# Optimization experiments

Hardware: AMD Instinct MI355X
Metric: run time of the kernel (lower is better)

The kernel has to match this reference:

```python
import jax, jax.numpy as jnp
import numpy as np

BN_EPS = 1e-5


def _weight_mlp(off, Wh, bh, Wo, bo):
    # off: [Nout, k, 2] relative neighbor offsets -> [Nout, k, 9] interp coeffs
    h = jax.nn.relu(off @ Wh + bh)
    return h @ Wo + bo


def _interp_conv(x, idx, off, Wk, bk, Wh, bh, Wo, bo):
    # x: [B, Cin, Nin]; idx: [Nout, k] neighbor indices into Nin; Wk: [Cout, Cin, 9]
    a = _weight_mlp(off, Wh, bh, Wo, bo)        # [Nout, k, 9]
    feats = x[:, :, idx]                         # gather -> [B, Cin, Nout, k]
    # dynamic filter: per-neighbor kernel = a @ Wk taps, contracted with features
    y = jnp.einsum('nkt,bcnk,oct->bon', a, feats, Wk)  # [B, Cout, Nout]
    return y + bk[None, :, None]


def _bn_relu(x, g, b):
    # BatchNorm1d over [B, C, N] using batch statistics (training-mode forward)
    mean = x.mean(axis=(0, 2), keepdims=True)
    var = x.var(axis=(0, 2), keepdims=True)
    xn = (x - mean) * jax.lax.rsqrt(var + BN_EPS)
    return jax.nn.relu(xn * g[None, :, None] + b[None, :, None])


def setup_inputs() -> dict:
    key = jax.random.key(0)
    ks = jax.random.split(key, 12)
    B, N1, N2, N3, K = 8, 50176, 12544, 3136, 9
    inp = {
        'x': jax.random.normal(ks[0], (B, 3, N1), jnp.float32),
        'nbr1': jax.random.randint(ks[1], (N2, K), 0, N1, jnp.int32),
        'off1': jax.random.normal(ks[2], (N2, K, 2), jnp.float32),
        'nbr2': jax.random.randint(ks[3], (N2, K), 0, N2, jnp.int32),
        'off2': jax.random.normal(ks[4], (N2, K, 2), jnp.float32),
        'pool_idx': jax.random.randint(ks[5], (N3, K), 0, N2, jnp.int32),
        'Wh': jax.random.normal(ks[6], (2, 32), jnp.float32) * 0.5,
        'bh': jnp.zeros((32,), jnp.float32),
        'Wo': jax.random.normal(ks[7], (32, 9), jnp.float32) * 0.2,
        'bo': jnp.zeros((9,), jnp.float32),
        'W1': jax.random.normal(ks[8], (32, 3, 9), jnp.float32) * 0.2,
        'b1': jnp.zeros((32,), jnp.float32),
        'W2': jax.random.normal(ks[9], (32, 32, 9), jnp.float32) * 0.06,
        'b2': jnp.zeros((32,), jnp.float32),
        'W3': jax.random.normal(ks[10], (64, 32, 9), jnp.float32) * 0.06,
        'b3': jnp.zeros((64,), jnp.float32),
        'g1': jnp.ones((32,), jnp.float32), 'be1': jnp.zeros((32,), jnp.float32),
        'g2': jnp.ones((32,), jnp.float32), 'be2': jnp.zeros((32,), jnp.float32),
        'g3': jnp.ones((64,), jnp.float32), 'be3': jnp.zeros((64,), jnp.float32),
    }
    return inp


def reference(x, nbr1, off1, nbr2, off2, pool_idx, Wh, bh, Wo, bo,
              W1, b1, W2, b2, W3, b3, g1, be1, g2, be2, g3, be3):
    x = _bn_relu(_interp_conv(x, nbr1, off1, W1, b1, Wh, bh, Wo, bo), g1, be1)
    x = _bn_relu(_interp_conv(x, nbr2, off2, W2, b2, Wh, bh, Wo, bo), g2, be2)
    x = _bn_relu(_interp_conv(x, nbr2, off2, W3, b3, Wh, bh, Wo, bo), g3, be3)
    # MaxPoolNG: max over irregular neighbor sets from level l2 -> l3
    x = x[:, :, pool_idx].max(axis=-1)           # [B, 64, N3]
    return x
```

## Files before the change

### kernel.cpp

```cpp
#include <hip/hip_runtime.h>
#include <math.h>

#define N1C 50176
#define N2C 12544
#define N3C 3136
#define NT_TILES (N2C * 8 / 64)

typedef __attribute__((ext_vector_type(8))) short bf16x8;
typedef __attribute__((ext_vector_type(4))) float f32x4;
typedef __attribute__((ext_vector_type(2))) unsigned uint2v;

__device__ __forceinline__ unsigned short f2bf(float f) {
    unsigned u = __builtin_bit_cast(unsigned, f);
    u += 0x7fffu + ((u >> 16) & 1u);
    return (unsigned short)(u >> 16);
}
__device__ __forceinline__ unsigned packbf(float a, float b) {
    return (unsigned)f2bf(a) | ((unsigned)f2bf(b) << 16);
}
__device__ __forceinline__ float bf2f(unsigned short u) {
    return __builtin_bit_cast(float, (unsigned)u << 16);
}
__device__ __forceinline__ float bflo(unsigned u) {
    return __builtin_bit_cast(float, u << 16);
}
__device__ __forceinline__ float bfhi(unsigned u) {
    return __builtin_bit_cast(float, u & 0xffff0000u);
}

#define TRB (N1C / 64)
#define MLB (2 * N2C * 9 / 256)
#define PWB 112

__device__ __forceinline__ void pad_one(int i, const float* __restrict__ W,
                                        unsigned short* __restrict__ Wp,
                                        int OC, int CIN, int KT) {
    int j = i & 7;
    int op = (i >> 3) & 31;
    int q = (i >> 8) & 3;
    int kt = (i >> 10) % KT;
    int g = i / (KT * 1024);
    int kp = kt * 32 + q * 8 + j;
    int t = kp / CIN, c = kp - t * CIN;
    int o = g * 32 + op;
    float v = (t < 9 && o < OC) ? W[(o * CIN + c) * 9 + t] : 0.f;
    Wp[i] = f2bf(v);
}

__global__ void prologue_kernel(const float* __restrict__ x, unsigned short* __restrict__ X0,
                                const float* __restrict__ off1, const float* __restrict__ off2,
                                const float* __restrict__ Wh, const float* __restrict__ bh,
                                const float* __restrict__ Wo, const float* __restrict__ bo,
                                float* __restrict__ A1, float* __restrict__ A2,
                                const float* __restrict__ W1, const float* __restrict__ W2,
                                const float* __restrict__ W3,
                                unsigned short* __restrict__ W1p, unsigned short* __restrict__ W2p,
                                unsigned short* __restrict__ W3p) {
    __shared__ float T[64][25];
    int blk = blockIdx.x;
    int tid = threadIdx.x;
    if (blk < TRB) {
        int n0 = blk * 64;
        for (int r = tid; r < 24 * 64; r += 256) {
            int cb = r >> 6;
            int nn = r & 63;
            T[nn][cb] = x[cb * N1C + n0 + nn];
        }
        __syncthreads();
        for (int w = tid; w < 64 * 24; w += 256) {
            int nn = w / 24;
            int u = w - nn * 24;
            X0[(n0 + nn) * 24 + u] = f2bf(T[nn][u]);
        }
    } else if (blk < TRB + MLB) {
        int idx = (blk - TRB) * 256 + tid;
        const float* offp;
        float* Ap;
        if (idx < N2C * 9) { offp = off1 + idx * 2; Ap = A1 + idx * 9; }
        else { int i2 = idx - N2C * 9; offp = off2 + i2 * 2; Ap = A2 + i2 * 9; }
        float o0 = offp[0], o1 = offp[1];
        float out[9];
#pragma unroll
        for (int t = 0; t < 9; t++) out[t] = bo[t];
#pragma unroll
        for (int h = 0; h < 32; h++) {
            float hv = fmaxf(o0 * Wh[h] + o1 * Wh[32 + h] + bh[h], 0.f);
#pragma unroll
            for (int t = 0; t < 9; t++) out[t] += hv * Wo[h * 9 + t];
        }
#pragma unroll
        for (int t = 0; t < 9; t++) Ap[t] = out[t];
    } else {
        int i = (blk - TRB - MLB) * 256 + tid;
        if (i < 1024) pad_one(i, W1, W1p, 32, 3, 1);
        else if (i < 10240) pad_one(i - 1024, W2, W2p, 32, 32, 9);
        else pad_one(i - 10240, W3, W3p, 64, 32, 9);
    }
}

__global__ __launch_bounds__(256, 8)
void conv1_kernel(const unsigned short* __restrict__ Xin,
                  const int* __restrict__ nbr,
                  const float* __restrict__ A,
                  const unsigned short* __restrict__ Wp,
                  const float* __restrict__ bias,
                  unsigned short* __restrict__ Yb) {
    constexpr int KSTR = 40;
    __shared__ alignas(16) short S[64 * KSTR];
    int tid = threadIdx.x;
    int n0 = blockIdx.x * 8;
    for (int i = tid; i < 64 * KSTR; i += 256) S[i] = 0;
    __syncthreads();
    if (tid < 192) {
        int nsub = tid / 24;
        int u = tid - nsub * 24;
        int b = u / 3, c = u - b * 3;
        int n = n0 + nsub;
        const int* nb = nbr + n * 9;
        const float* Ar = A + n * 81;
        float f[9];
#pragma unroll
        for (int k = 0; k < 9; k++) f[k] = bf2f(Xin[nb[k] * 24 + u]);
        float s[9];
#pragma unroll
        for (int t = 0; t < 9; t++) s[t] = 0.f;
#pragma unroll
        for (int k = 0; k < 9; k++)
#pragma unroll
            for (int t = 0; t < 9; t++) s[t] = fmaf(Ar[k * 9 + t], f[k], s[t]);
        int col = nsub * 8 + b;
#pragma unroll
        for (int t = 0; t < 9; t++) S[col * KSTR + t * 3 + c] = (short)f2bf(s[t]);
    }
    __syncthreads();
    int lane = tid & 63, wv = tid >> 6, q = lane >> 4, cl = lane & 15;
    int colg = wv * 16 + cl;
    const bf16x8* wf = (const bf16x8*)Wp;
    f32x4 acc0 = {0.f, 0.f, 0.f, 0.f};
    f32x4 acc1 = {0.f, 0.f, 0.f, 0.f};
    bf16x8 bfr = *(const bf16x8*)&S[colg * KSTR + q * 8];
    bf16x8 a0 = wf[q * 32 + cl];
    bf16x8 a1 = wf[q * 32 + cl + 16];
    acc0 = __builtin_amdgcn_mfma_f32_16x16x32_bf16(a0, bfr, acc0, 0, 0, 0);
    acc1 = __builtin_amdgcn_mfma_f32_16x16x32_bf16(a1, bfr, acc1, 0, 0, 0);
    int C = blockIdx.x * 64 + colg;
#pragma unroll
    for (int m = 0; m < 2; m++) {
        f32x4 ac = m ? acc1 : acc0;
        int ob = m * 16 + q * 4;
        uint2v uu;
        uu.x = packbf(ac[0] + bias[ob + 0], ac[1] + bias[ob + 1]);
        uu.y = packbf(ac[2] + bias[ob + 2], ac[3] + bias[ob + 3]);
        *(uint2v*)&Yb[(size_t)C * 32 + ob] = uu;
    }
}

#define KSTR32 296

template <int MW, bool HAS_BN>
__global__ __launch_bounds__(256, 8)
void conv32_kernel(const unsigned short* __restrict__ Xin,
                   const int* __restrict__ nbr,
                   const float* __restrict__ A,
                   const unsigned short* __restrict__ Wp,
                   const float* __restrict__ bias,
                   const float* __restrict__ bnsc,
                   const float* __restrict__ bnsh,
                   unsigned short* __restrict__ Yb) {
    constexpr int OC = MW * 16;
    constexpr int MPW = MW / 2;
    __shared__ alignas(16) short S[32 * KSTR32];

    int tid = threadIdx.x;
    int n0 = blockIdx.x * 4;
    int nsel = __builtin_amdgcn_readfirstlane(tid >> 7);
    int rem = tid & 127;
    int b = rem >> 4, c2 = rem & 15;
    float sc0 = 1.f, sh0 = 0.f, sc1 = 1.f, sh1 = 0.f;
    if (HAS_BN) {
        sc0 = bnsc[2 * c2]; sc1 = bnsc[2 * c2 + 1];
        sh0 = bnsh[2 * c2]; sh1 = bnsh[2 * c2 + 1];
    }
    const unsigned* Xu = (const unsigned*)Xin;

    unsigned fu[18];
#pragma unroll
    for (int g = 0; g < 2; g++)
#pragma unroll
        for (int k = 0; k < 9; k++) {
            int j = nbr[(n0 + nsel * 2 + g) * 9 + k];
            fu[g * 9 + k] = Xu[(size_t)j * 128 + rem];
        }
#pragma unroll
    for (int g = 0; g < 2; g++) {
        const float* Ar = A + (n0 + nsel * 2 + g) * 81;
        float s0[9], s1[9];
#pragma unroll
        for (int t = 0; t < 9; t++) { s0[t] = 0.f; s1[t] = 0.f; }
#pragma unroll
        for (int k = 0; k < 9; k++) {
            unsigned u = fu[g * 9 + k];
            float lo = bflo(u), hi = bfhi(u);
            if (HAS_BN) {
                lo = fmaxf(fmaf(lo, sc0, sh0), 0.f);
                hi = fmaxf(fmaf(hi, sc1, sh1), 0.f);
            }
#pragma unroll
            for (int t = 0; t < 9; t++) {
                float a = Ar[k * 9 + t];
                s0[t] = fmaf(a, lo, s0[t]);
                s1[t] = fmaf(a, hi, s1[t]);
            }
        }
        int col = (nsel * 2 + g) * 8 + b;
        unsigned* Srow = (unsigned*)&S[col * KSTR32];
#pragma unroll
        for (int t = 0; t < 9; t++) Srow[t * 16 + c2] = packbf(s0[t], s1[t]);
    }
    __syncthreads();

    int lane = tid & 63, wv = tid >> 6, q = lane >> 4, cl = lane & 15;
    int colg = (wv & 1) * 16 + cl;
    int mbase = (wv >> 1) * MPW;
    const bf16x8* wf = (const bf16x8*)Wp;
    f32x4 acc[MPW];
#pragma unroll
    for (int mi = 0; mi < MPW; mi++) acc[mi] = (f32x4){0.f, 0.f, 0.f, 0.f};
#pragma unroll
    for (int kt = 0; kt < 9; kt++) {
        bf16x8 bfr = *(const bf16x8*)&S[colg * KSTR32 + kt * 32 + q * 8];
#pragma unroll
        for (int mi = 0; mi < MPW; mi++) {
            int m = mbase + mi;
            const bf16x8* wg = wf + (m >> 1) * (9 * 128);
            bf16x8 am = wg[(kt * 4 + q) * 32 + cl + (m & 1) * 16];
            acc[mi] = __builtin_amdgcn_mfma_f32_16x16x32_bf16(am, bfr, acc[mi], 0, 0, 0);
        }
    }
    int C = blockIdx.x * 32 + colg;
#pragma unroll
    for (int mi = 0; mi < MPW; mi++) {
        int ob = (mbase + mi) * 16 + q * 4;
        uint2v uu;
        uu.x = packbf(acc[mi][0] + bias[ob + 0], acc[mi][1] + bias[ob + 1]);
        uu.y = packbf(acc[mi][2] + bias[ob + 2], acc[mi][3] + bias[ob + 3]);
        *(uint2v*)&Yb[(size_t)C * OC + ob] = uu;
    }
}

template <int OC>
__global__ __launch_bounds__(256, 8)
void bn_sum(const unsigned short* __restrict__ Yb, double* __restrict__ Part) {
    constexpr int CLS = OC / 2;
    constexpr int TOTU = N2C * 8 * OC / 2;
    const unsigned* Yu = (const unsigned*)Yb;
    int tid = threadIdx.x;
    double s0 = 0, q0 = 0, s1 = 0, q1 = 0;
    for (int p = blockIdx.x * 256 + tid; p < TOTU; p += 128 * 256) {
        unsigned u = Yu[p];
        double lo = (double)bflo(u), hi = (double)bfhi(u);
        s0 += lo; q0 += lo * lo;
        s1 += hi; q1 += hi * hi;
    }
#pragma unroll
    for (int d = CLS; d < 64; d <<= 1) {
        s0 += __shfl_xor(s0, d); q0 += __shfl_xor(q0, d);
        s1 += __shfl_xor(s1, d); q1 += __shfl_xor(q1, d);
    }
    __shared__ double red[4][CLS][4];
    int wv = tid >> 6, lane = tid & 63;
    if (lane < CLS) {
        red[wv][lane][0] = s0; red[wv][lane][1] = q0;
        red[wv][lane][2] = s1; red[wv][lane][3] = q1;
    }
    __syncthreads();
    if (tid < 2 * OC) {
        int o = (tid < OC) ? tid : tid - OC;
        int isq = (tid >= OC) ? 1 : 0;
        int cls = o >> 1, slot = (o & 1) * 2 + isq;
        double v = red[0][cls][slot] + red[1][cls][slot] + red[2][cls][slot] + red[3][cls][slot];
        Part[(size_t)tid * 128 + blockIdx.x] = v;
    }
}

__global__ void bn_fin(const double* __restrict__ Part,
                       const float* __restrict__ g, const float* __restrict__ be,
                       float* __restrict__ sc, float* __restrict__ sh, int OC) {
    int o = blockIdx.x;
    int t = threadIdx.x;
    double s = Part[(size_t)o * 128 + t] + Part[(size_t)o * 128 + t + 64];
    double q = Part[(size_t)(OC + o) * 128 + t] + Part[(size_t)(OC + o) * 128 + t + 64];
#pragma unroll
    for (int d = 1; d < 64; d <<= 1) {
        s += __shfl_xor(s, d);
        q += __shfl_xor(q, d);
    }
    if (t == 0) {
        double cnt = (double)N2C * 8.0;
        double mean = s / cnt;
        double var = q / cnt - mean * mean;
        double rs = 1.0 / sqrt(var + 1e-5);
        double scale = (double)g[o] * rs;
        sc[o] = (float)scale;
        sh[o] = (float)((double)be[o] - mean * scale);
    }
}

__global__ __launch_bounds__(512, 4)
void pool_kernel(const unsigned short* __restrict__ Y3, const int* __restrict__ pidx,
                 const float* __restrict__ sc, const float* __restrict__ sh,
                 float* __restrict__ out) {
    int m0 = blockIdx.x * 8;
    int tid = threadIdx.x;
    int o = tid & 63;
    float s = sc[o], h = sh[o];
    float mx[8];
    int jn[9];
#pragma unroll
    for (int k = 0; k < 9; k++) jn[k] = pidx[m0 * 9 + k];
#pragma unroll 1
    for (int mi = 0; mi < 8; mi++) {
        int jc[9];
#pragma unroll
        for (int k = 0; k < 9; k++) jc[k] = jn[k];
        if (mi < 7) {
#pragma unroll
            for (int k = 0; k < 9; k++) jn[k] = pidx[(m0 + mi + 1) * 9 + k];
        }
        float v0 = 0.f;
#pragma unroll
        for (int k = 0; k < 9; k++) {
            float v = bf2f(Y3[(size_t)jc[k] * 512 + tid]);
            v0 = fmaxf(v0, fmaf(v, s, h));
        }
        mx[mi] = fmaxf(v0, 0.f);
    }
    float* op = out + (size_t)tid * 3136 + m0;
#pragma unroll
    for (int mi = 0; mi < 8; mi++) op[mi] = mx[mi];
}

extern "C" void kernel_launch(void* const* d_in, const int* in_sizes, int n_in,
                              void* d_out, int out_size, void* d_ws, size_t ws_size,
                              hipStream_t stream) {
    const float* x    = (const float*)d_in[0];
    const int*   nbr1 = (const int*)d_in[1];
    const float* off1 = (const float*)d_in[2];
    const int*   nbr2 = (const int*)d_in[3];
    const float* off2 = (const float*)d_in[4];
    const int*   pidx = (const int*)d_in[5];
    const float* Wh   = (const float*)d_in[6];
    const float* bh   = (const float*)d_in[7];
    const float* Wo   = (const float*)d_in[8];
    const float* bo   = (const float*)d_in[9];
    const float* W1   = (const float*)d_in[10];
    const float* b1   = (const float*)d_in[11];
    const float* W2   = (const float*)d_in[12];
    const float* b2   = (const float*)d_in[13];
    const float* W3   = (const float*)d_in[14];
    const float* b3   = (const float*)d_in[15];
    const float* g1   = (const float*)d_in[16];
    const float* be1  = (const float*)d_in[17];
    const float* g2   = (const float*)d_in[18];
    const float* be2  = (const float*)d_in[19];
    const float* g3   = (const float*)d_in[20];
    const float* be3  = (const float*)d_in[21];

    char* ws = (char*)d_ws;
    size_t off = 0;
    auto alloc = [&](size_t bytes) -> void* {
        void* p = ws + off;
        off += (bytes + 255) & ~(size_t)255;
        return p;
    };
    unsigned short* X0b = (unsigned short*)alloc((size_t)N1C * 24 * 2);
    float* A1 = (float*)alloc((size_t)N2C * 81 * 4);
    float* A2 = (float*)alloc((size_t)N2C * 81 * 4);
    unsigned short* Y1b = (unsigned short*)alloc((size_t)N2C * 8 * 32 * 2);
    unsigned short* Y2b = (unsigned short*)alloc((size_t)N2C * 8 * 32 * 2);
    unsigned short* Y3b = (unsigned short*)alloc((size_t)N2C * 8 * 64 * 2);
    unsigned short* W1p = (unsigned short*)alloc(32 * 32 * 2);
    unsigned short* W2p = (unsigned short*)alloc(32 * 288 * 2);
    unsigned short* W3p = (unsigned short*)alloc(64 * 288 * 2);
    double* Part  = (double*)alloc(128 * 128 * 8);
    float*  scbuf = (float*)alloc(256 * 4);

    float* sc1 = scbuf;       float* sh1 = scbuf + 32;
    float* sc2 = scbuf + 64;  float* sh2 = scbuf + 96;
    float* sc3 = scbuf + 128; float* sh3 = scbuf + 192;

    prologue_kernel<<<TRB + MLB + PWB, 256, 0, stream>>>(
        x, X0b, off1, off2, Wh, bh, Wo, bo, A1, A2, W1, W2, W3, W1p, W2p, W3p);

    conv1_kernel<<<NT_TILES, 256, 0, stream>>>(X0b, nbr1, A1, W1p, b1, Y1b);
    bn_sum<32><<<128, 256, 0, stream>>>(Y1b, Part);
    bn_fin<<<32, 64, 0, stream>>>(Part, g1, be1, sc1, sh1, 32);

    conv32_kernel<2, true><<<N2C / 4, 256, 0, stream>>>(
        Y1b, nbr2, A2, W2p, b2, sc1, sh1, Y2b);
    bn_sum<32><<<128, 256, 0, stream>>>(Y2b, Part);
    bn_fin<<<32, 64, 0, stream>>>(Part, g2, be2, sc2, sh2, 32);

    conv32_kernel<4, true><<<N2C / 4, 256, 0, stream>>>(
        Y2b, nbr2, A2, W3p, b3, sc2, sh2, Y3b);
    bn_sum<64><<<128, 256, 0, stream>>>(Y3b, Part);
    bn_fin<<<64, 64, 0, stream>>>(Part, g3, be3, sc3, sh3, 64);

    pool_kernel<<<N3C / 8, 512, 0, stream>>>(Y3b, pidx, sc3, sh3, (float*)d_out);
}
```

Before: 227.9 us.

## Make each wave own its tile in conv kernels, replacing block barriers with wave sync

```diff
diff --git a/kernel.cpp b/kernel.cpp
--- a/kernel.cpp
+++ b/kernel.cpp
@@ -9,6 +9,9 @@
 typedef __attribute__((ext_vector_type(8))) short bf16x8;
 typedef __attribute__((ext_vector_type(4))) float f32x4;
 typedef __attribute__((ext_vector_type(2))) unsigned uint2v;
+
+#define WAVE_SYNC()  do { __builtin_amdgcn_fence(__ATOMIC_ACQ_REL, "wavefront"); \
+                          __builtin_amdgcn_wave_barrier(); } while (0)
 
 __device__ __forceinline__ unsigned short f2bf(float f) {
     unsigned u = __builtin_bit_cast(unsigned, f);
@@ -98,7 +101,7 @@
     }
 }
 
-__global__ __launch_bounds__(256, 8)
+__global__ __launch_bounds__(256, 4)
 void conv1_kernel(const unsigned short* __restrict__ Xin,
                   const int* __restrict__ nbr,
                   const float* __restrict__ A,
@@ -106,16 +109,22 @@
                   const float* __restrict__ bias,
                   unsigned short* __restrict__ Yb) {
     constexpr int KSTR = 40;
-    __shared__ alignas(16) short S[64 * KSTR];
+    __shared__ alignas(16) short S[4][16 * KSTR];
     int tid = threadIdx.x;
-    int n0 = blockIdx.x * 8;
-    for (int i = tid; i < 64 * KSTR; i += 256) S[i] = 0;
-    __syncthreads();
-    if (tid < 192) {
-        int nsub = tid / 24;
-        int u = tid - nsub * 24;
+    int w = __builtin_amdgcn_readfirstlane(tid >> 6);
+    int lane = tid & 63;
+    short* Sw = &S[w][0];
+    unsigned* Sz = (unsigned*)Sw;
+#pragma unroll
+    for (int i = 0; i < 5; i++) Sz[lane + 64 * i] = 0;
+    WAVE_SYNC();
+
+    int nb0 = blockIdx.x * 8 + w * 2;
+    if (lane < 48) {
+        int g = lane / 24;
+        int u = lane - g * 24;
         int b = u / 3, c = u - b * 3;
-        int n = n0 + nsub;
+        int n = nb0 + g;
         const int* nb = nbr + n * 9;
         const float* Ar = A + n * 81;
         float f[9];
@@ -128,22 +137,21 @@
         for (int k = 0; k < 9; k++)
 #pragma unroll
             for (int t = 0; t < 9; t++) s[t] = fmaf(Ar[k * 9 + t], f[k], s[t]);
-        int col = nsub * 8 + b;
-#pragma unroll
-        for (int t = 0; t < 9; t++) S[col * KSTR + t * 3 + c] = (short)f2bf(s[t]);
-    }
-    __syncthreads();
-    int lane = tid & 63, wv = tid >> 6, q = lane >> 4, cl = lane & 15;
-    int colg = wv * 16 + cl;
+        int col = g * 8 + b;
+#pragma unroll
+        for (int t = 0; t < 9; t++) Sw[col * KSTR + t * 3 + c] = (short)f2bf(s[t]);
+    }
+    WAVE_SYNC();
+    int q = lane >> 4, cl = lane & 15;
     const bf16x8* wf = (const bf16x8*)Wp;
     f32x4 acc0 = {0.f, 0.f, 0.f, 0.f};
     f32x4 acc1 = {0.f, 0.f, 0.f, 0.f};
-    bf16x8 bfr = *(const bf16x8*)&S[colg * KSTR + q * 8];
+    bf16x8 bfr = *(const bf16x8*)&Sw[cl * KSTR + q * 8];
     bf16x8 a0 = wf[q * 32 + cl];
     bf16x8 a1 = wf[q * 32 + cl + 16];
     acc0 = __builtin_amdgcn_mfma_f32_16x16x32_bf16(a0, bfr, acc0, 0, 0, 0);
     acc1 = __builtin_amdgcn_mfma_f32_16x16x32_bf16(a1, bfr, acc1, 0, 0, 0);
-    int C = blockIdx.x * 64 + colg;
+    int C = blockIdx.x * 64 + w * 16 + cl;
 #pragma unroll
     for (int m = 0; m < 2; m++) {
         f32x4 ac = m ? acc1 : acc0;
@@ -155,10 +163,8 @@
     }
 }
 
-#define KSTR32 296
-
 template <int MW, bool HAS_BN>
-__global__ __launch_bounds__(256, 8)
+__global__ __launch_bounds__(256, 4)
 void conv32_kernel(const unsigned short* __restrict__ Xin,
                    const int* __restrict__ nbr,
                    const float* __restrict__ A,
@@ -168,82 +174,84 @@
                    const float* __restrict__ bnsh,
                    unsigned short* __restrict__ Yb) {
     constexpr int OC = MW * 16;
-    constexpr int MPW = MW / 2;
-    __shared__ alignas(16) short S[32 * KSTR32];
-
+    constexpr int KSTR = 296;
+    __shared__ alignas(16) short S[4][16 * KSTR];
     int tid = threadIdx.x;
-    int n0 = blockIdx.x * 4;
-    int nsel = __builtin_amdgcn_readfirstlane(tid >> 7);
-    int rem = tid & 127;
-    int b = rem >> 4, c2 = rem & 15;
-    float sc0 = 1.f, sh0 = 0.f, sc1 = 1.f, sh1 = 0.f;
+    int w = __builtin_amdgcn_readfirstlane(tid >> 6);
+    int lane = tid & 63;
+    short* Sw = &S[w][0];
+    int b = lane >> 3, c4 = lane & 7;
+    int nb0 = blockIdx.x * 8 + w * 2;
+
+    float sc[4], sh[4];
     if (HAS_BN) {
-        sc0 = bnsc[2 * c2]; sc1 = bnsc[2 * c2 + 1];
-        sh0 = bnsh[2 * c2]; sh1 = bnsh[2 * c2 + 1];
-    }
-    const unsigned* Xu = (const unsigned*)Xin;
-
-    unsigned fu[18];
+#pragma unroll
+        for (int i = 0; i < 4; i++) { sc[i] = bnsc[4 * c4 + i]; sh[i] = bnsh[4 * c4 + i]; }
+    }
+    const uint2v* Xu2 = (const uint2v*)Xin;
+
+    uint2v fu[2][9];
 #pragma unroll
     for (int g = 0; g < 2; g++)
 #pragma unroll
         for (int k = 0; k < 9; k++) {
-            int j = nbr[(n0 + nsel * 2 + g) * 9 + k];
-            fu[g * 9 + k] = Xu[(size_t)j * 128 + rem];
+            int j = nbr[(nb0 + g) * 9 + k];
+            fu[g][k] = Xu2[(size_t)(j * 8 + b) * 8 + c4];
         }
 #pragma unroll
     for (int g = 0; g < 2; g++) {
-        const float* Ar = A + (n0 + nsel * 2 + g) * 81;
-        float s0[9], s1[9];
-#pragma unroll
-        for (int t = 0; t < 9; t++) { s0[t] = 0.f; s1[t] = 0.f; }
+        const float* Ar = A + (nb0 + g) * 81;
+        float s[9][4];
+#pragma unroll
+        for (int t = 0; t < 9; t++)
+#pragma unroll
+            for (int i = 0; i < 4; i++) s[t][i] = 0.f;
 #pragma unroll
         for (int k = 0; k < 9; k++) {
-            unsigned u = fu[g * 9 + k];
-            float lo = bflo(u), hi = bfhi(u);
+            uint2v u = fu[g][k];
+            float v[4] = {bflo(u.x), bfhi(u.x), bflo(u.y), bfhi(u.y)};
             if (HAS_BN) {
-                lo = fmaxf(fmaf(lo, sc0, sh0), 0.f);
-                hi = fmaxf(fmaf(hi, sc1, sh1), 0.f);
+#pragma unroll
+                for (int i = 0; i < 4; i++) v[i] = fmaxf(fmaf(v[i], sc[i], sh[i]), 0.f);
             }
 #pragma unroll
             for (int t = 0; t < 9; t++) {
                 float a = Ar[k * 9 + t];
-                s0[t] = fmaf(a, lo, s0[t]);
-                s1[t] = fmaf(a, hi, s1[t]);
+#pragma unroll
+                for (int i = 0; i < 4; i++) s[t][i] = fmaf(a, v[i], s[t][i]);
             }
         }
-        int col = (nsel * 2 + g) * 8 + b;
-        unsigned* Srow = (unsigned*)&S[col * KSTR32];
-#pragma unroll
-        for (int t = 0; t < 9; t++) Srow[t * 16 + c2] = packbf(s0[t], s1[t]);
-    }
-    __syncthreads();
-
-    int lane = tid & 63, wv = tid >> 6, q = lane >> 4, cl = lane & 15;
-    int colg = (wv & 1) * 16 + cl;
-    int mbase = (wv >> 1) * MPW;
+        unsigned* Srow = (unsigned*)&Sw[(g * 8 + b) * KSTR];
+#pragma unroll
+        for (int t = 0; t < 9; t++) {
+            uint2v p;
+            p.x = packbf(s[t][0], s[t][1]);
+            p.y = packbf(s[t][2], s[t][3]);
+            *(uint2v*)&Srow[t * 16 + 2 * c4] = p;
+        }
+    }
+    WAVE_SYNC();
+    int q = lane >> 4, cl = lane & 15;
     const bf16x8* wf = (const bf16x8*)Wp;
-    f32x4 acc[MPW];
-#pragma unroll
-    for (int mi = 0; mi < MPW; mi++) acc[mi] = (f32x4){0.f, 0.f, 0.f, 0.f};
+    f32x4 acc[MW];
+#pragma unroll
+    for (int m = 0; m < MW; m++) acc[m] = (f32x4){0.f, 0.f, 0.f, 0.f};
 #pragma unroll
     for (int kt = 0; kt < 9; kt++) {
-        bf16x8 bfr = *(const bf16x8*)&S[colg * KSTR32 + kt * 32 + q * 8];
-#pragma unroll
-        for (int mi = 0; mi < MPW; mi++) {
-            int m = mbase + mi;
-            const bf16x8* wg = wf + (m >> 1) * (9 * 128);
-            bf16x8 am = wg[(kt * 4 + q) * 32 + cl + (m & 1) * 16];
-            acc[mi] = __builtin_amdgcn_mfma_f32_16x16x32_bf16(am, bfr, acc[mi], 0, 0, 0);
-        }
-    }
-    int C = blockIdx.x * 32 + colg;
-#pragma unroll
-    for (int mi = 0; mi < MPW; mi++) {
-        int ob = (mbase + mi) * 16 + q * 4;
+        bf16x8 bfr = *(const bf16x8*)&Sw[cl * KSTR + kt * 32 + q * 8];
+#pragma unroll
+        for (int m = 0; m < MW; m++) {
+            bf16x8 am = wf[(m >> 1) * (9 * 128) + (kt * 4 + q) * 32 + cl + (m & 1) * 16];
+            acc[m] = __builtin_amdgcn_mfma_f32_16x16x32_bf16(am, bfr, acc[m], 0, 0, 0);
+        }
+    }
+    int C = blockIdx.x * 64 + w * 16 + cl;
+#pragma unroll
+    for (int m = 0; m < MW; m++) {
+        int ob = m * 16 + q * 4;
         uint2v uu;
-        uu.x = packbf(acc[mi][0] + bias[ob + 0], acc[mi][1] + bias[ob + 1]);
-        uu.y = packbf(acc[mi][2] + bias[ob + 2], acc[mi][3] + bias[ob + 3]);
+        uu.x = packbf(acc[m][0] + bias[ob + 0], acc[m][1] + bias[ob + 1]);
+        uu.y = packbf(acc[m][2] + bias[ob + 2], acc[m][3] + bias[ob + 3]);
         *(uint2v*)&Yb[(size_t)C * OC + ob] = uu;
     }
 }
@@ -396,12 +404,12 @@
     bn_sum<32><<<128, 256, 0, stream>>>(Y1b, Part);
     bn_fin<<<32, 64, 0, stream>>>(Part, g1, be1, sc1, sh1, 32);
 
-    conv32_kernel<2, true><<<N2C / 4, 256, 0, stream>>>(
+    conv32_kernel<2, true><<<NT_TILES, 256, 0, stream>>>(
         Y1b, nbr2, A2, W2p, b2, sc1, sh1, Y2b);
     bn_sum<32><<<128, 256, 0, stream>>>(Y2b, Part);
     bn_fin<<<32, 64, 0, stream>>>(Part, g2, be2, sc2, sh2, 32);
 
-    conv32_kernel<4, true><<<N2C / 4, 256, 0, stream>>>(
+    conv32_kernel<4, true><<<NT_TILES, 256, 0, stream>>>(
         Y2b, nbr2, A2, W3p, b3, sc2, sh2, Y3b);
     bn_sum<64><<<128, 256, 0, stream>>>(Y3b, Part);
     bn_fin<<<64, 64, 0, stream>>>(Part, g3, be3, sc3, sh3, 64);
```

Measured after the change: 228.0 us. No clear change (+0.1%).
